# Kernel tuning notes

Hardware: AMD Instinct MI355X
Metric: run time of the kernel (lower is better)

The kernel has to match this reference:

```python
import jax, jax.numpy as jnp
import numpy as np

N = 65536  # number of points
# (out_ch, in_ch) for the 8 shared-MLP (1x1-conv) blocks
_DIMS = [(64, 3), (64, 64), (128, 64), (1024, 128), (512, 1088), (256, 512), (128, 256), (1, 128)]


def setup_inputs() -> dict:
    key = jax.random.key(0)
    ks = jax.random.split(key, 1 + 2 * len(_DIMS))
    inp = {"x": jax.random.normal(ks[0], (1, 1, N, 3), jnp.float32)}
    for i, (o, c) in enumerate(_DIMS):
        scale = 1.0 / np.sqrt(c)
        inp[f"W{i+1}"] = jax.random.normal(ks[1 + 2 * i], (o, c), jnp.float32) * scale
        inp[f"b{i+1}"] = jax.random.uniform(ks[2 + 2 * i], (o,), jnp.float32, -scale, scale)
    return inp


def reference(x, W1, b1, W2, b2, W3, b3, W4, b4, W5, b5, W6, b6, W7, b7, W8, b8):
    # x: [1,1,n,3]. Conv2d with kernel [1,3] over the width-3 axis == per-point linear on xyz.
    pts = x[0, 0]                                   # [n,3]
    n = pts.shape[0]
    h = jax.nn.relu(pts @ W1.T + b1)                # [n,64]   block1
    h = jax.nn.relu(h @ W2.T + b2)                  # [n,64]   block2 (kept for skip-concat)
    y = jax.nn.relu(h @ W3.T + b3)                  # [n,128]  block3
    y = jax.nn.relu(y @ W4.T + b4)                  # [n,1024] block4
    g = jnp.max(y, axis=0)                          # [1024]   global max-pool over points
    # broadcast global feature to every point and concat with per-point features -> [n,1088]
    feat = jnp.concatenate([h, jnp.broadcast_to(g, (n, g.shape[0]))], axis=1)
    z = jax.nn.relu(feat @ W5.T + b5)               # [n,512]
    z = jax.nn.relu(z @ W6.T + b6)                  # [n,256]
    z = jax.nn.relu(z @ W7.T + b7)                  # [n,128]
    z = z @ W8.T + b8                               # [n,1]    block8 (no relu)
    return z.reshape(1, 1, n, 1)
```

## Files before the change

kernel.cpp:

```cpp
#include <hip/hip_runtime.h>

#define NPTS 65536

typedef __bf16 bf16_t;
typedef __bf16 bf16x8 __attribute__((ext_vector_type(8)));
typedef float f32x16 __attribute__((ext_vector_type(16)));

#define MFMA32(A, B, C) __builtin_amdgcn_mfma_f32_32x32x16_bf16(A, B, C, 0, 0, 0)

__device__ __forceinline__ float relu(float v) { return v > 0.f ? v : 0.f; }


struct PrepSeg { const float* src; bf16_t* h; bf16_t* l; int SW; int K; int nblk; };
struct PrepAll { PrepSeg seg[6]; };

__global__ __launch_bounds__(256) void kprep(PrepAll pa) {
  int blk = blockIdx.x, i = 0;
  while (blk >= pa.seg[i].nblk) { blk -= pa.seg[i].nblk; ++i; }
  const PrepSeg sg = pa.seg[i];
  int t8 = blk * 256 + threadIdx.x;
  int l = t8 & 63;
  int rest = t8 >> 6;
  int NKC = sg.K >> 4;
  int kc = rest % NKC, st = rest / NKC;
  int n = st * 32 + (l & 31);
  int k0 = kc * 16 + (l >> 5) * 8;
  const float* src = sg.src + (size_t)n * sg.SW + k0;
  bf16x8 hv, lv;
#pragma unroll
  for (int j = 0; j < 8; ++j) {
    float v = src[j];
    bf16_t h = (bf16_t)v;
    hv[j] = h; lv[j] = (bf16_t)(v - (float)h);
  }
  *(bf16x8*)(sg.h + (size_t)t8 * 8) = hv;
  *(bf16x8*)(sg.l + (size_t)t8 * 8) = lv;
}

__global__ __launch_bounds__(256, 2) void k1a(
    const float* __restrict__ x, const float* __restrict__ W1, const float* __restrict__ b1,
    bf16_t* __restrict__ h1h, bf16_t* __restrict__ h1l) {
  int p = blockIdx.x * 256 + threadIdx.x;
  float x0 = x[p * 3 + 0], x1 = x[p * 3 + 1], x2 = x[p * 3 + 2];
  int b = p >> 7, mi = (p >> 5) & 3, p31 = p & 31;
#pragma unroll
  for (int kc = 0; kc < 4; ++kc)
#pragma unroll
    for (int hbw = 0; hbw < 2; ++hbw) {
      bf16x8 hv, lv;
#pragma unroll
      for (int j = 0; j < 8; ++j) {
        int c = kc * 16 + hbw * 8 + j;
        float v = relu(fmaf(W1[c * 3], x0, fmaf(W1[c * 3 + 1], x1, fmaf(W1[c * 3 + 2], x2, b1[c]))));
        bf16_t h = (bf16_t)v;
        hv[j] = h; lv[j] = (bf16_t)(v - (float)h);
      }
      size_t off = (((size_t)(b * 4 + kc) * 4 + mi) * 64 + hbw * 32 + p31) * 8;
      *(bf16x8*)(h1h + off) = hv;
      *(bf16x8*)(h1l + off) = lv;
    }
}

template <int PB, int K, int MODE>
__global__ __launch_bounds__(256, 3) void gemmS(
    const bf16_t* __restrict__ Ah, const bf16_t* __restrict__ Al,
    const bf16_t* __restrict__ Wh, const bf16_t* __restrict__ Wl,
    const float* __restrict__ bias, int nko,
    bf16_t* __restrict__ Oh, bf16_t* __restrict__ Ol,
    float* __restrict__ aux, const float* __restrict__ w8, const float* __restrict__ b8) {
  constexpr int WC = 4 / PB;
  constexpr int NKC = K / 16;
  constexpr int KG = 2;
  constexpr int NG = NKC / KG;
  __shared__ bf16_t smem[2][PB][2][KG * 2048];

  int tid = threadIdx.x;
  int lane = tid & 63;
  int w = __builtin_amdgcn_readfirstlane(tid >> 6);
  int rg = w / WC, cw = w % WC;
  int hb = lane >> 5, p31 = lane & 31;
  int bx = blockIdx.x;
  int st0 = blockIdx.y * WC + cw;
  int bblk = bx * PB + rg;

  f32x16 acc[4];
#pragma unroll
  for (int r = 0; r < 16; ++r) {
    float bv = bias[st0 * 32 + 8 * (r >> 2) + 4 * hb + (r & 3)];
#pragma unroll
    for (int mi = 0; mi < 4; ++mi) acc[mi][r] = bv;
  }

  auto stage = [&](int buf, int g) {
#pragma unroll
    for (int i = 0; i < PB * 4; ++i) {
      int u = i * 256 + tid;
      int rgs = u >> 10, rem = u & 1023;
      int t = rem >> 9, inner = rem & 511;
      const bf16_t* src = (t ? Al : Ah) +
          ((size_t)(bx * PB + rgs) * NKC + g * KG) * 2048 + inner * 8;
      *(bf16x8*)&smem[buf][rgs][t][inner * 8] = *(const bf16x8*)src;
    }
  };

  bf16x8 wch[KG], wcl[KG], wnh[KG], wnl[KG];
  auto wload = [&](int g, bf16x8* h, bf16x8* l) {
#pragma unroll
    for (int kcl = 0; kcl < KG; ++kcl) {
      size_t wo = (((size_t)st0 * NKC + g * KG + kcl) * 64 + lane) * 8;
      h[kcl] = *(const bf16x8*)(Wh + wo);
      l[kcl] = *(const bf16x8*)(Wl + wo);
    }
  };

  auto compute = [&](int buf, bf16x8* h, bf16x8* l) {
#pragma unroll
    for (int kcl = 0; kcl < KG; ++kcl)
#pragma unroll
      for (int mi = 0; mi < 4; ++mi) {
        const bf16_t* xp = &smem[buf][rg][0][((kcl * 4 + mi) * 64 + lane) * 8];
        bf16x8 xh = *(const bf16x8*)xp;
        bf16x8 xl = *(const bf16x8*)(xp + KG * 2048);
        acc[mi] = MFMA32(h[kcl], xh, acc[mi]);
        acc[mi] = MFMA32(l[kcl], xh, acc[mi]);
        acc[mi] = MFMA32(h[kcl], xl, acc[mi]);
      }
  };

  stage(0, 0);
  wload(0, wch, wcl);
  for (int g = 0; g < NG; ++g) {
    __syncthreads();
    if (g + 1 < NG) {
      stage((g + 1) & 1, g + 1);
      wload(g + 1, wnh, wnl);
    }
    compute(g & 1, wch, wcl);
#pragma unroll
    for (int kcl = 0; kcl < KG; ++kcl) { wch[kcl] = wnh[kcl]; wcl[kcl] = wnl[kcl]; }
  }

  if constexpr (MODE == 0) {
#pragma unroll
    for (int mi = 0; mi < 4; ++mi) {
      float a[16], rcv[8];
#pragma unroll
      for (int r = 0; r < 16; ++r) a[r] = relu(acc[mi][r]);
#pragma unroll
      for (int j = 0; j < 8; ++j) rcv[j] = __shfl_xor(hb ? a[j] : a[8 + j], 32);
      float o0[8], o1[8];
#pragma unroll
      for (int j = 0; j < 4; ++j) {
        o0[j]     = hb ? rcv[j]     : a[j];
        o0[4 + j] = hb ? a[8 + j]   : rcv[j];
        o1[j]     = hb ? rcv[4 + j] : a[4 + j];
        o1[4 + j] = hb ? a[12 + j]  : rcv[4 + j];
      }
      bf16x8 h0, l0, h1, l1;
#pragma unroll
      for (int j = 0; j < 8; ++j) {
        bf16_t x0 = (bf16_t)o0[j]; h0[j] = x0; l0[j] = (bf16_t)(o0[j] - (float)x0);
        bf16_t x1 = (bf16_t)o1[j]; h1[j] = x1; l1[j] = (bf16_t)(o1[j] - (float)x1);
      }
      int kco = st0 * 2 + hb;
      size_t ob = ((size_t)(bblk * nko + kco) * 4 + mi) * 64;
      *(bf16x8*)(Oh + (ob + p31) * 8)      = h0;
      *(bf16x8*)(Ol + (ob + p31) * 8)      = l0;
      *(bf16x8*)(Oh + (ob + 32 + p31) * 8) = h1;
      *(bf16x8*)(Ol + (ob + 32 + p31) * 8) = l1;
    }
  } else if constexpr (MODE == 1) {
#pragma unroll
    for (int r = 0; r < 16; ++r) {
      float m = relu(acc[0][r]);
#pragma unroll
      for (int mi = 1; mi < 4; ++mi) m = fmaxf(m, relu(acc[mi][r]));
#pragma unroll
      for (int off = 1; off < 32; off <<= 1) m = fmaxf(m, __shfl_xor(m, off));
      if (p31 == 0)
        aux[(size_t)bx * 1024 + st0 * 32 + 8 * (r >> 2) + 4 * hb + (r & 3)] = m;
    }
  } else {
    __shared__ float sp[4][128];
    float w8v[16];
#pragma unroll
    for (int r = 0; r < 16; ++r) w8v[r] = w8[st0 * 32 + 8 * (r >> 2) + 4 * hb + (r & 3)];
#pragma unroll
    for (int mi = 0; mi < 4; ++mi) {
      float s = 0.f;
#pragma unroll
      for (int r = 0; r < 16; ++r) s = fmaf(relu(acc[mi][r]), w8v[r], s);
      s += __shfl_xor(s, 32);
      if (hb == 0) sp[w][mi * 32 + p31] = s;
    }
    __syncthreads();
    if (tid < 128)
      aux[(size_t)bx * 128 + tid] = sp[0][tid] + sp[1][tid] + sp[2][tid] + sp[3][tid] + b8[0];
  }
}

__global__ __launch_bounds__(256) void kgmax(const float* __restrict__ gpart, float* __restrict__ g) {
  int t = blockIdx.x * 256 + threadIdx.x;
  int c = t & 1023, rg = t >> 10;
  const float* gp = gpart + (size_t)rg * 64 * 1024 + c;
  float m = 0.f;
#pragma unroll 8
  for (int r = 0; r < 64; ++r) m = fmaxf(m, gp[(size_t)r * 1024]);
  atomicMax((unsigned int*)(g + c), __float_as_uint(m));
}

__global__ __launch_bounds__(256) void kc5(
    const float* __restrict__ W5, const float* __restrict__ b5,
    const float* __restrict__ g, float* __restrict__ c5) {
  int tid = threadIdx.x;
  int ci = tid >> 3, kg = tid & 7;
  int c = blockIdx.x * 32 + ci;
  const float* wrow = W5 + (size_t)c * 1088 + 64 + kg * 128;
  const float* gp = g + kg * 128;
  float acc = 0.f;
#pragma unroll 8
  for (int k = 0; k < 128; ++k) acc += wrow[k] * gp[k];
#pragma unroll
  for (int off = 1; off <= 4; off <<= 1) acc += __shfl_xor(acc, off);
  if (kg == 0) c5[c] = acc + b5[c];
}


struct Oct { bf16x8 h0, l0, h1, l1; };
__device__ __forceinline__ Oct epi_pack(const f32x16& accv, int hb) {
  float a[16], rcv[8];
#pragma unroll
  for (int r = 0; r < 16; ++r) a[r] = relu(accv[r]);
#pragma unroll
  for (int j = 0; j < 8; ++j) rcv[j] = __shfl_xor(hb ? a[j] : a[8 + j], 32);
  float o0[8], o1[8];
#pragma unroll
  for (int j = 0; j < 4; ++j) {
    o0[j]     = hb ? rcv[j]     : a[j];
    o0[4 + j] = hb ? a[8 + j]   : rcv[j];
    o1[j]     = hb ? rcv[4 + j] : a[4 + j];
    o1[4 + j] = hb ? a[12 + j]  : rcv[4 + j];
  }
  Oct o;
#pragma unroll
  for (int j = 0; j < 8; ++j) {
    bf16_t x0 = (bf16_t)o0[j]; o.h0[j] = x0; o.l0[j] = (bf16_t)(o0[j] - (float)x0);
    bf16_t x1 = (bf16_t)o1[j]; o.h1[j] = x1; o.l1[j] = (bf16_t)(o1[j] - (float)x1);
  }
  return o;
}

__device__ __forceinline__ void epi_store_lds(const Oct& o, bf16_t* H, bf16_t* L, int ob, int p31) {
  *(bf16x8*)(H + (ob + p31) * 8)      = o.h0;
  *(bf16x8*)(H + (ob + 32 + p31) * 8) = o.h1;
  *(bf16x8*)(L + (ob + p31) * 8)      = o.l0;
  *(bf16x8*)(L + (ob + 32 + p31) * 8) = o.l1;
}

__device__ __forceinline__ void binit2(f32x16 acc[2], const float* bias, int base, int hb) {
#pragma unroll
  for (int r = 0; r < 16; ++r) {
    float bv = bias[base + 8 * (r >> 2) + 4 * hb + (r & 3)];
    acc[0][r] = bv; acc[1][r] = bv;
  }
}

template <int NKC>
__device__ __forceinline__ void wgemm(const bf16_t* __restrict__ Wh, const bf16_t* __restrict__ Wl,
                                      int st, const bf16_t* act, int loOff, int lane,
                                      f32x16 acc[2]) {
#pragma unroll
  for (int kc = 0; kc < NKC; ++kc) {
    size_t wo = ((size_t)(st * NKC + kc) * 64 + lane) * 8;
    bf16x8 awh = *(const bf16x8*)(Wh + wo), awl = *(const bf16x8*)(Wl + wo);
    bf16x8 xh[2], xl[2];
#pragma unroll
    for (int mi = 0; mi < 2; ++mi) {
      const bf16_t* xp = act + ((kc * 2 + mi) * 64 + lane) * 8;
      xh[mi] = *(const bf16x8*)xp; xl[mi] = *(const bf16x8*)(xp + loOff);
    }
#pragma unroll
    for (int mi = 0; mi < 2; ++mi) acc[mi] = MFMA32(awh, xh[mi], acc[mi]);
#pragma unroll
    for (int mi = 0; mi < 2; ++mi) acc[mi] = MFMA32(awl, xh[mi], acc[mi]);
#pragma unroll
    for (int mi = 0; mi < 2; ++mi) acc[mi] = MFMA32(awh, xl[mi], acc[mi]);
  }
}

__global__ __launch_bounds__(256, 2) void mega2(
    const bf16_t* __restrict__ h2gh, const bf16_t* __restrict__ h2gl,
    const bf16_t* __restrict__ W5h, const bf16_t* __restrict__ W5l, const float* __restrict__ c5,
    const bf16_t* __restrict__ W6h, const bf16_t* __restrict__ W6l, const float* __restrict__ b6,
    const bf16_t* __restrict__ W7h, const bf16_t* __restrict__ W7l, const float* __restrict__ b7,
    const float* __restrict__ w8, const float* __restrict__ b8v, float* __restrict__ out) {
  __shared__ __align__(16) bf16_t smem[32768];
  __shared__ float sp[4][64];
  int tid = threadIdx.x, lane = tid & 63;
  int w = __builtin_amdgcn_readfirstlane(tid >> 6);
  int hb = lane >> 5, p31 = lane & 31;
  int b = blockIdx.x;
  int B = b >> 1, half = b & 1;
  bf16_t* z5buf = smem + 8192;

#pragma unroll
  for (int i = 0; i < 4; ++i) {
    int u = i * 256 + tid;
    int t = u >> 9, rem = u & 511;
    int kcmi = rem >> 6, l = rem & 63;
    int kc = kcmi >> 1, mi2 = kcmi & 1;
    size_t so = ((size_t)((B * 4 + kc) * 4 + half * 2 + mi2) * 64 + l) * 8;
    const bf16_t* src = (t ? h2gl : h2gh) + so;
    *(bf16x8*)(smem + t * 4096 + rem * 8) = *(const bf16x8*)src;
  }
  __syncthreads();

  f32x16 z6a[2][2];
#pragma unroll
  for (int s = 0; s < 2; ++s)
#pragma unroll
    for (int r = 0; r < 16; ++r) {
      float bv = b6[(w * 2 + s) * 32 + 8 * (r >> 2) + 4 * hb + (r & 3)];
      z6a[s][0][r] = bv; z6a[s][1][r] = bv;
    }

  for (int g5 = 0; g5 < 4; ++g5) {
    int st5 = g5 * 4 + w;
    f32x16 a5[2];
    binit2(a5, c5, st5 * 32, hb);
    wgemm<4>(W5h, W5l, st5, smem, 4096, lane, a5);
    __syncthreads();
#pragma unroll
    for (int mi = 0; mi < 2; ++mi) {
      Oct o = epi_pack(a5[mi], hb);
      epi_store_lds(o, z5buf, z5buf + 8192, ((w * 2 + hb) * 2 + mi) * 64, p31);
    }
    __syncthreads();
#pragma unroll
    for (int kc = 0; kc < 8; ++kc) {
      bf16x8 awh[2], awl[2], xh[2], xl[2];
#pragma unroll
      for (int s = 0; s < 2; ++s) {
        size_t wo = ((size_t)((w * 2 + s) * 32 + g5 * 8 + kc) * 64 + lane) * 8;
        awh[s] = *(const bf16x8*)(W6h + wo);
        awl[s] = *(const bf16x8*)(W6l + wo);
      }
#pragma unroll
      for (int mi = 0; mi < 2; ++mi) {
        const bf16_t* xp = z5buf + ((kc * 2 + mi) * 64 + lane) * 8;
        xh[mi] = *(const bf16x8*)xp; xl[mi] = *(const bf16x8*)(xp + 8192);
      }
#pragma unroll
      for (int s = 0; s < 2; ++s)
#pragma unroll
        for (int mi = 0; mi < 2; ++mi) z6a[s][mi] = MFMA32(awh[s], xh[mi], z6a[s][mi]);
#pragma unroll
      for (int s = 0; s < 2; ++s)
#pragma unroll
        for (int mi = 0; mi < 2; ++mi) z6a[s][mi] = MFMA32(awl[s], xh[mi], z6a[s][mi]);
#pragma unroll
      for (int s = 0; s < 2; ++s)
#pragma unroll
        for (int mi = 0; mi < 2; ++mi) z6a[s][mi] = MFMA32(awh[s], xl[mi], z6a[s][mi]);
    }
  }
  __syncthreads();
#pragma unroll
  for (int s = 0; s < 2; ++s) {
    int kcb = (w * 2 + s) * 2 + hb;
#pragma unroll
    for (int mi = 0; mi < 2; ++mi) {
      Oct o = epi_pack(z6a[s][mi], hb);
      epi_store_lds(o, smem, smem + 16384, (kcb * 2 + mi) * 64, p31);
    }
  }
  __syncthreads();
  f32x16 a7[2];
  binit2(a7, b7, w * 32, hb);
  wgemm<16>(W7h, W7l, w, smem, 16384, lane, a7);
  float w8v[16];
#pragma unroll
  for (int r = 0; r < 16; ++r) w8v[r] = w8[w * 32 + 8 * (r >> 2) + 4 * hb + (r & 3)];
#pragma unroll
  for (int mi = 0; mi < 2; ++mi) {
    float s = 0.f;
#pragma unroll
    for (int r = 0; r < 16; ++r) s = fmaf(relu(a7[mi][r]), w8v[r], s);
    s += __shfl_xor(s, 32);
    if (hb == 0) sp[w][mi * 32 + p31] = s;
  }
  __syncthreads();
  if (tid < 64)
    out[b * 64 + tid] = sp[0][tid] + sp[1][tid] + sp[2][tid] + sp[3][tid] + b8v[0];
}

extern "C" void kernel_launch(void* const* d_in, const int* in_sizes, int n_in,
                              void* d_out, int out_size, void* d_ws, size_t ws_size,
                              hipStream_t stream) {
  const float* x  = (const float*)d_in[0];
  const float* W1 = (const float*)d_in[1];  const float* b1 = (const float*)d_in[2];
  const float* W2 = (const float*)d_in[3];  const float* b2 = (const float*)d_in[4];
  const float* W3 = (const float*)d_in[5];  const float* b3 = (const float*)d_in[6];
  const float* W4 = (const float*)d_in[7];  const float* b4 = (const float*)d_in[8];
  const float* W5 = (const float*)d_in[9];  const float* b5 = (const float*)d_in[10];
  const float* W6 = (const float*)d_in[11]; const float* b6 = (const float*)d_in[12];
  const float* W7 = (const float*)d_in[13]; const float* b7 = (const float*)d_in[14];
  const float* W8 = (const float*)d_in[15]; const float* b8 = (const float*)d_in[16];
  float* out = (float*)d_out;

  const size_t MB = 1ull << 20;
  char* ws = (char*)d_ws;
  bf16_t* h2h = (bf16_t*)(ws + 128 * MB);  bf16_t* h2l = (bf16_t*)(ws + 136 * MB);
  bf16_t* h1h = (bf16_t*)(ws + 144 * MB);  bf16_t* h1l = (bf16_t*)(ws + 152 * MB);
  bf16_t* y3h = (bf16_t*)(ws + 144 * MB);  bf16_t* y3l = (bf16_t*)(ws + 160 * MB);
  float* gpart = (float*)(ws + 208 * MB);
  float* g     = (float*)(ws + 210 * MB);
  float* c5    = (float*)(ws + 210 * MB + 4096);
  char* wb = ws + 210 * MB + 65536;
  bf16_t* W2h = (bf16_t*)(wb);             bf16_t* W2l = (bf16_t*)(wb + 8192);
  bf16_t* W3h = (bf16_t*)(wb + 16384);     bf16_t* W3l = (bf16_t*)(wb + 32768);
  bf16_t* W4h = (bf16_t*)(wb + 49152);     bf16_t* W4l = (bf16_t*)(wb + 311296);
  bf16_t* W5h = (bf16_t*)(wb + 573440);    bf16_t* W5l = (bf16_t*)(wb + 638976);
  bf16_t* W6h = (bf16_t*)(wb + 704512);    bf16_t* W6l = (bf16_t*)(wb + 966656);
  bf16_t* W7h = (bf16_t*)(wb + 1228800);   bf16_t* W7l = (bf16_t*)(wb + 1294336);

  hipMemsetAsync(g, 0, 1024 * sizeof(float), stream);

  PrepAll pa;
  pa.seg[0] = {W2, W2h, W2l, 64, 64, 2};
  pa.seg[1] = {W3, W3h, W3l, 64, 64, 4};
  pa.seg[2] = {W4, W4h, W4l, 128, 128, 64};
  pa.seg[3] = {W5, W5h, W5l, 1088, 64, 16};
  pa.seg[4] = {W6, W6h, W6l, 512, 512, 64};
  pa.seg[5] = {W7, W7h, W7l, 256, 256, 16};
  kprep<<<166, 256, 0, stream>>>(pa);

  k1a<<<256, 256, 0, stream>>>(x, W1, b1, h1h, h1l);
  gemmS<2, 64, 0><<<dim3(256, 1), 256, 0, stream>>>(
      h1h, h1l, W2h, W2l, b2, 4, h2h, h2l, nullptr, nullptr, nullptr);
  gemmS<1, 64, 0><<<dim3(512, 1), 256, 0, stream>>>(
      h2h, h2l, W3h, W3l, b3, 8, y3h, y3l, nullptr, nullptr, nullptr);
  gemmS<1, 128, 1><<<dim3(512, 8), 256, 0, stream>>>(
      y3h, y3l, W4h, W4l, b4, 0, nullptr, nullptr, gpart, nullptr, nullptr);
  kgmax<<<32, 256, 0, stream>>>(gpart, g);
  kc5<<<16, 256, 0, stream>>>(W5, b5, g, c5);
  mega2<<<1024, 256, 0, stream>>>(h2h, h2l, W5h, W5l, c5, W6h, W6l, b6,
                                  W7h, W7l, b7, W8, b8, out);
}
```

Measured before the change: 305.7 us.

## Add dedicated layer-4 max kernel and software-pipeline weight loads in mega2

```diff
diff --git a/kernel.cpp b/kernel.cpp
--- a/kernel.cpp
+++ b/kernel.cpp
@@ -199,6 +199,71 @@
   }
 }
 
+__global__ __launch_bounds__(256, 2) void kl4max(
+    const bf16_t* __restrict__ Ah, const bf16_t* __restrict__ Al,
+    const bf16_t* __restrict__ Wh, const bf16_t* __restrict__ Wl,
+    const float* __restrict__ bias, float* __restrict__ gpart) {
+  __shared__ __align__(16) bf16_t sA[32768];
+  int tid = threadIdx.x, lane = tid & 63;
+  int w = __builtin_amdgcn_readfirstlane(tid >> 6);
+  int hb = lane >> 5, p31 = lane & 31;
+  int bx = blockIdx.x;
+  const bf16_t* srcH = Ah + (size_t)bx * 16384;
+  const bf16_t* srcL = Al + (size_t)bx * 16384;
+#pragma unroll
+  for (int i = 0; i < 8; ++i) {
+    int u = i * 256 + tid;
+    *(bf16x8*)(sA + (size_t)u * 8)         = *(const bf16x8*)(srcH + (size_t)u * 8);
+    *(bf16x8*)(sA + 16384 + (size_t)u * 8) = *(const bf16x8*)(srcL + (size_t)u * 8);
+  }
+  __syncthreads();
+
+  for (int j = 0; j < 8; ++j) {
+    int st = j * 4 + w;
+    bf16x8 wh[8], wl[8];
+#pragma unroll
+    for (int kc = 0; kc < 8; ++kc) {
+      size_t wo = ((size_t)(st * 8 + kc) * 64 + lane) * 8;
+      wh[kc] = *(const bf16x8*)(Wh + wo);
+      wl[kc] = *(const bf16x8*)(Wl + wo);
+    }
+    f32x16 acc[4];
+#pragma unroll
+    for (int r = 0; r < 16; ++r) {
+      float bv = bias[st * 32 + 8 * (r >> 2) + 4 * hb + (r & 3)];
+#pragma unroll
+      for (int mi = 0; mi < 4; ++mi) acc[mi][r] = bv;
+    }
+#pragma unroll
+    for (int kc = 0; kc < 8; ++kc) {
+      bf16x8 xh[4], xl[4];
+#pragma unroll
+      for (int mi = 0; mi < 4; ++mi) {
+        const bf16_t* xp = sA + ((kc * 4 + mi) * 64 + lane) * 8;
+        xh[mi] = *(const bf16x8*)xp;
+        xl[mi] = *(const bf16x8*)(xp + 16384);
+      }
+      __builtin_amdgcn_s_setprio(1);
+#pragma unroll
+      for (int mi = 0; mi < 4; ++mi) acc[mi] = MFMA32(wh[kc], xh[mi], acc[mi]);
+#pragma unroll
+      for (int mi = 0; mi < 4; ++mi) acc[mi] = MFMA32(wl[kc], xh[mi], acc[mi]);
+#pragma unroll
+      for (int mi = 0; mi < 4; ++mi) acc[mi] = MFMA32(wh[kc], xl[mi], acc[mi]);
+      __builtin_amdgcn_s_setprio(0);
+    }
+#pragma unroll
+    for (int r = 0; r < 16; ++r) {
+      float m = fmaxf(fmaxf(acc[0][r], acc[1][r]), fmaxf(acc[2][r], acc[3][r]));
+      m = fmaxf(m, 0.f);
+#pragma unroll
+      for (int off = 1; off < 32; off <<= 1) m = fmaxf(m, __shfl_xor(m, off));
+      if (p31 == 0)
+        gpart[(size_t)bx * 1024 + st * 32 + 8 * (r >> 2) + 4 * hb + (r & 3)] = m;
+    }
+  }
+}
+
 __global__ __launch_bounds__(256) void kgmax(const float* __restrict__ gpart, float* __restrict__ g) {
   int t = blockIdx.x * 256 + threadIdx.x;
   int c = t & 1023, rg = t >> 10;
@@ -262,29 +327,6 @@
   for (int r = 0; r < 16; ++r) {
     float bv = bias[base + 8 * (r >> 2) + 4 * hb + (r & 3)];
     acc[0][r] = bv; acc[1][r] = bv;
-  }
-}
-
-template <int NKC>
-__device__ __forceinline__ void wgemm(const bf16_t* __restrict__ Wh, const bf16_t* __restrict__ Wl,
-                                      int st, const bf16_t* act, int loOff, int lane,
-                                      f32x16 acc[2]) {
-#pragma unroll
-  for (int kc = 0; kc < NKC; ++kc) {
-    size_t wo = ((size_t)(st * NKC + kc) * 64 + lane) * 8;
-    bf16x8 awh = *(const bf16x8*)(Wh + wo), awl = *(const bf16x8*)(Wl + wo);
-    bf16x8 xh[2], xl[2];
-#pragma unroll
-    for (int mi = 0; mi < 2; ++mi) {
-      const bf16_t* xp = act + ((kc * 2 + mi) * 64 + lane) * 8;
-      xh[mi] = *(const bf16x8*)xp; xl[mi] = *(const bf16x8*)(xp + loOff);
-    }
-#pragma unroll
-    for (int mi = 0; mi < 2; ++mi) acc[mi] = MFMA32(awh, xh[mi], acc[mi]);
-#pragma unroll
-    for (int mi = 0; mi < 2; ++mi) acc[mi] = MFMA32(awl, xh[mi], acc[mi]);
-#pragma unroll
-    for (int mi = 0; mi < 2; ++mi) acc[mi] = MFMA32(awh, xl[mi], acc[mi]);
   }
 }
 
@@ -301,19 +343,16 @@
   int hb = lane >> 5, p31 = lane & 31;
   int b = blockIdx.x;
   int B = b >> 1, half = b & 1;
-  bf16_t* z5buf = smem + 8192;
-
-#pragma unroll
-  for (int i = 0; i < 4; ++i) {
-    int u = i * 256 + tid;
-    int t = u >> 9, rem = u & 511;
-    int kcmi = rem >> 6, l = rem & 63;
-    int kc = kcmi >> 1, mi2 = kcmi & 1;
-    size_t so = ((size_t)((B * 4 + kc) * 4 + half * 2 + mi2) * 64 + l) * 8;
-    const bf16_t* src = (t ? h2gl : h2gh) + so;
-    *(bf16x8*)(smem + t * 4096 + rem * 8) = *(const bf16x8*)src;
-  }
-  __syncthreads();
+
+  bf16x8 xh[4][2], xl[4][2];
+#pragma unroll
+  for (int kc = 0; kc < 4; ++kc)
+#pragma unroll
+    for (int mi = 0; mi < 2; ++mi) {
+      size_t so = (((size_t)((B * 4 + kc) * 4 + half * 2 + mi)) * 64 + lane) * 8;
+      xh[kc][mi] = *(const bf16x8*)(h2gh + so);
+      xl[kc][mi] = *(const bf16x8*)(h2gl + so);
+    }
 
   f32x16 z6a[2][2];
 #pragma unroll
@@ -324,44 +363,77 @@
       z6a[s][0][r] = bv; z6a[s][1][r] = bv;
     }
 
+  bf16x8 w5h[4], w5l[4];
+  auto w5load = [&](int g) {
+#pragma unroll
+    for (int kc = 0; kc < 4; ++kc) {
+      size_t wo = (((size_t)(g * 4 + w) * 4 + kc) * 64 + lane) * 8;
+      w5h[kc] = *(const bf16x8*)(W5h + wo);
+      w5l[kc] = *(const bf16x8*)(W5l + wo);
+    }
+  };
+  w5load(0);
+
+  bf16x8 cwh[2], cwl[2], nwh[2], nwl[2];
+  auto w6load = [&](int g, int kc, bf16x8* hh, bf16x8* ll) {
+#pragma unroll
+    for (int s = 0; s < 2; ++s) {
+      size_t wo = ((size_t)((w * 2 + s) * 32 + g * 8 + kc) * 64 + lane) * 8;
+      hh[s] = *(const bf16x8*)(W6h + wo);
+      ll[s] = *(const bf16x8*)(W6l + wo);
+    }
+  };
+
   for (int g5 = 0; g5 < 4; ++g5) {
+    bf16_t* zbuf = smem + (g5 & 1) * 16384;
     int st5 = g5 * 4 + w;
     f32x16 a5[2];
     binit2(a5, c5, st5 * 32, hb);
-    wgemm<4>(W5h, W5l, st5, smem, 4096, lane, a5);
-    __syncthreads();
+    __builtin_amdgcn_s_setprio(1);
+#pragma unroll
+    for (int kc = 0; kc < 4; ++kc) {
+#pragma unroll
+      for (int mi = 0; mi < 2; ++mi) a5[mi] = MFMA32(w5h[kc], xh[kc][mi], a5[mi]);
+#pragma unroll
+      for (int mi = 0; mi < 2; ++mi) a5[mi] = MFMA32(w5l[kc], xh[kc][mi], a5[mi]);
+#pragma unroll
+      for (int mi = 0; mi < 2; ++mi) a5[mi] = MFMA32(w5h[kc], xl[kc][mi], a5[mi]);
+    }
+    __builtin_amdgcn_s_setprio(0);
+    if (g5 < 3) w5load(g5 + 1);
 #pragma unroll
     for (int mi = 0; mi < 2; ++mi) {
       Oct o = epi_pack(a5[mi], hb);
-      epi_store_lds(o, z5buf, z5buf + 8192, ((w * 2 + hb) * 2 + mi) * 64, p31);
-    }
+      epi_store_lds(o, zbuf, zbuf + 8192, ((w * 2 + hb) * 2 + mi) * 64, p31);
+    }
+    w6load(g5, 0, cwh, cwl);
     __syncthreads();
 #pragma unroll
     for (int kc = 0; kc < 8; ++kc) {
-      bf16x8 awh[2], awl[2], xh[2], xl[2];
-#pragma unroll
-      for (int s = 0; s < 2; ++s) {
-        size_t wo = ((size_t)((w * 2 + s) * 32 + g5 * 8 + kc) * 64 + lane) * 8;
-        awh[s] = *(const bf16x8*)(W6h + wo);
-        awl[s] = *(const bf16x8*)(W6l + wo);
+      if (kc < 7) w6load(g5, kc + 1, nwh, nwl);
+      bf16x8 zxh[2], zxl[2];
+#pragma unroll
+      for (int mi = 0; mi < 2; ++mi) {
+        const bf16_t* xp = zbuf + ((kc * 2 + mi) * 64 + lane) * 8;
+        zxh[mi] = *(const bf16x8*)xp;
+        zxl[mi] = *(const bf16x8*)(xp + 8192);
       }
-#pragma unroll
-      for (int mi = 0; mi < 2; ++mi) {
-        const bf16_t* xp = z5buf + ((kc * 2 + mi) * 64 + lane) * 8;
-        xh[mi] = *(const bf16x8*)xp; xl[mi] = *(const bf16x8*)(xp + 8192);
-      }
+      __builtin_amdgcn_s_setprio(1);
 #pragma unroll
       for (int s = 0; s < 2; ++s)
 #pragma unroll
-        for (int mi = 0; mi < 2; ++mi) z6a[s][mi] = MFMA32(awh[s], xh[mi], z6a[s][mi]);
+        for (int mi = 0; mi < 2; ++mi) z6a[s][mi] = MFMA32(cwh[s], zxh[mi], z6a[s][mi]);
 #pragma unroll
       for (int s = 0; s < 2; ++s)
 #pragma unroll
-        for (int mi = 0; mi < 2; ++mi) z6a[s][mi] = MFMA32(awl[s], xh[mi], z6a[s][mi]);
+        for (int mi = 0; mi < 2; ++mi) z6a[s][mi] = MFMA32(cwl[s], zxh[mi], z6a[s][mi]);
 #pragma unroll
       for (int s = 0; s < 2; ++s)
 #pragma unroll
-        for (int mi = 0; mi < 2; ++mi) z6a[s][mi] = MFMA32(awh[s], xl[mi], z6a[s][mi]);
+        for (int mi = 0; mi < 2; ++mi) z6a[s][mi] = MFMA32(cwh[s], zxl[mi], z6a[s][mi]);
+      __builtin_amdgcn_s_setprio(0);
+#pragma unroll
+      for (int s = 0; s < 2; ++s) { cwh[s] = nwh[s]; cwl[s] = nwl[s]; }
     }
   }
   __syncthreads();
@@ -374,10 +446,39 @@
       epi_store_lds(o, smem, smem + 16384, (kcb * 2 + mi) * 64, p31);
     }
   }
+  bf16x8 a7wh, a7wl, n7h, n7l;
+  {
+    size_t wo = ((size_t)(w * 16) * 64 + lane) * 8;
+    a7wh = *(const bf16x8*)(W7h + wo);
+    a7wl = *(const bf16x8*)(W7l + wo);
+  }
   __syncthreads();
   f32x16 a7[2];
   binit2(a7, b7, w * 32, hb);
-  wgemm<16>(W7h, W7l, w, smem, 16384, lane, a7);
+#pragma unroll
+  for (int kc = 0; kc < 16; ++kc) {
+    if (kc < 15) {
+      size_t wo = ((size_t)(w * 16 + kc + 1) * 64 + lane) * 8;
+      n7h = *(const bf16x8*)(W7h + wo);
+      n7l = *(const bf16x8*)(W7l + wo);
+    }
+    bf16x8 zxh[2], zxl[2];
+#pragma unroll
+    for (int mi = 0; mi < 2; ++mi) {
+      const bf16_t* xp = smem + ((kc * 2 + mi) * 64 + lane) * 8;
+      zxh[mi] = *(const bf16x8*)xp;
+      zxl[mi] = *(const bf16x8*)(xp + 16384);
+    }
+    __builtin_amdgcn_s_setprio(1);
+#pragma unroll
+    for (int mi = 0; mi < 2; ++mi) a7[mi] = MFMA32(a7wh, zxh[mi], a7[mi]);
+#pragma unroll
+    for (int mi = 0; mi < 2; ++mi) a7[mi] = MFMA32(a7wl, zxh[mi], a7[mi]);
+#pragma unroll
+    for (int mi = 0; mi < 2; ++mi) a7[mi] = MFMA32(a7wh, zxl[mi], a7[mi]);
+    __builtin_amdgcn_s_setprio(0);
+    a7wh = n7h; a7wl = n7l;
+  }
   float w8v[16];
 #pragma unroll
   for (int r = 0; r < 16; ++r) w8v[r] = w8[w * 32 + 8 * (r >> 2) + 4 * hb + (r & 3)];
@@ -440,8 +541,7 @@
       h1h, h1l, W2h, W2l, b2, 4, h2h, h2l, nullptr, nullptr, nullptr);
   gemmS<1, 64, 0><<<dim3(512, 1), 256, 0, stream>>>(
       h2h, h2l, W3h, W3l, b3, 8, y3h, y3l, nullptr, nullptr, nullptr);
-  gemmS<1, 128, 1><<<dim3(512, 8), 256, 0, stream>>>(
-      y3h, y3l, W4h, W4l, b4, 0, nullptr, nullptr, gpart, nullptr, nullptr);
+  kl4max<<<512, 256, 0, stream>>>(y3h, y3l, W4h, W4l, b4, gpart);
   kgmax<<<32, 256, 0, stream>>>(gpart, g);
   kc5<<<16, 256, 0, stream>>>(W5, b5, g, c5);
   mega2<<<1024, 256, 0, stream>>>(h2h, h2l, W5h, W5l, c5, W6h, W6l, b6,
```

New measurement: 380.5 us. 24.4% more time.

## Replace layer-4 GEMM+max with dedicated kernel keeping activation tile in LDS

Applied to the files above, without the earlier changes.

```diff
diff --git a/kernel.cpp b/kernel.cpp
--- a/kernel.cpp
+++ b/kernel.cpp
@@ -196,6 +196,72 @@
     __syncthreads();
     if (tid < 128)
       aux[(size_t)bx * 128 + tid] = sp[0][tid] + sp[1][tid] + sp[2][tid] + sp[3][tid] + b8[0];
+  }
+}
+
+__global__ __launch_bounds__(256, 2) void kl4max(
+    const bf16_t* __restrict__ Ah, const bf16_t* __restrict__ Al,
+    const bf16_t* __restrict__ Wh, const bf16_t* __restrict__ Wl,
+    const float* __restrict__ bias, float* __restrict__ gpart) {
+  __shared__ __align__(16) bf16_t sA[32768];
+  int tid = threadIdx.x, lane = tid & 63;
+  int w = __builtin_amdgcn_readfirstlane(tid >> 6);
+  int hb = lane >> 5, p31 = lane & 31;
+  int bx = blockIdx.x;
+  const bf16_t* srcH = Ah + (size_t)bx * 16384;
+  const bf16_t* srcL = Al + (size_t)bx * 16384;
+#pragma unroll
+  for (int i = 0; i < 8; ++i) {
+    int u = i * 256 + tid;
+    *(bf16x8*)(sA + (size_t)u * 8)         = *(const bf16x8*)(srcH + (size_t)u * 8);
+    *(bf16x8*)(sA + 16384 + (size_t)u * 8) = *(const bf16x8*)(srcL + (size_t)u * 8);
+  }
+  __syncthreads();
+
+  for (int j = 0; j < 8; ++j) {
+    int st = j * 4 + w;
+    bf16x8 cwh, cwl, nwh, nwl;
+    {
+      size_t wo = ((size_t)(st * 8) * 64 + lane) * 8;
+      cwh = *(const bf16x8*)(Wh + wo);
+      cwl = *(const bf16x8*)(Wl + wo);
+    }
+    f32x16 acc[4];
+#pragma unroll
+    for (int r = 0; r < 16; ++r) {
+      float bv = bias[st * 32 + 8 * (r >> 2) + 4 * hb + (r & 3)];
+#pragma unroll
+      for (int mi = 0; mi < 4; ++mi) acc[mi][r] = bv;
+    }
+#pragma unroll
+    for (int kc = 0; kc < 8; ++kc) {
+      if (kc < 7) {
+        size_t wo = ((size_t)(st * 8 + kc + 1) * 64 + lane) * 8;
+        nwh = *(const bf16x8*)(Wh + wo);
+        nwl = *(const bf16x8*)(Wl + wo);
+      }
+      __builtin_amdgcn_s_setprio(1);
+#pragma unroll
+      for (int mi = 0; mi < 4; ++mi) {
+        const bf16_t* xp = sA + ((kc * 4 + mi) * 64 + lane) * 8;
+        bf16x8 xh = *(const bf16x8*)xp;
+        bf16x8 xl = *(const bf16x8*)(xp + 16384);
+        acc[mi] = MFMA32(cwh, xh, acc[mi]);
+        acc[mi] = MFMA32(cwl, xh, acc[mi]);
+        acc[mi] = MFMA32(cwh, xl, acc[mi]);
+      }
+      __builtin_amdgcn_s_setprio(0);
+      cwh = nwh; cwl = nwl;
+    }
+#pragma unroll
+    for (int r = 0; r < 16; ++r) {
+      float m = fmaxf(fmaxf(acc[0][r], acc[1][r]), fmaxf(acc[2][r], acc[3][r]));
+      m = fmaxf(m, 0.f);
+#pragma unroll
+      for (int off = 1; off < 32; off <<= 1) m = fmaxf(m, __shfl_xor(m, off));
+      if (p31 == 0)
+        gpart[(size_t)bx * 1024 + st * 32 + 8 * (r >> 2) + 4 * hb + (r & 3)] = m;
+    }
   }
 }
 
@@ -440,8 +506,7 @@
       h1h, h1l, W2h, W2l, b2, 4, h2h, h2l, nullptr, nullptr, nullptr);
   gemmS<1, 64, 0><<<dim3(512, 1), 256, 0, stream>>>(
       h2h, h2l, W3h, W3l, b3, 8, y3h, y3l, nullptr, nullptr, nullptr);
-  gemmS<1, 128, 1><<<dim3(512, 8), 256, 0, stream>>>(
-      y3h, y3l, W4h, W4l, b4, 0, nullptr, nullptr, gpart, nullptr, nullptr);
+  kl4max<<<512, 256, 0, stream>>>(y3h, y3l, W4h, W4l, b4, gpart);
   kgmax<<<32, 256, 0, stream>>>(gpart, g);
   kc5<<<16, 256, 0, stream>>>(W5, b5, g, c5);
   mega2<<<1024, 256, 0, stream>>>(h2h, h2l, W5h, W5l, c5, W6h, W6l, b6,
```

Result: slower. 347.2 us (+13.5%).
